# Performance work log

Hardware: AMD Instinct MI355X
Metric: run time of the kernel (lower is better)

Reference implementation:

```python
import jax, jax.numpy as jnp
import numpy as np

B, T, XS, HS = 256, 512, 256, 256


def setup_inputs() -> dict:
    key = jax.random.key(0)
    ks = jax.random.split(key, 9)
    scale_x = np.sqrt(6.0 / (XS + HS)).astype(np.float32)  # xavier_uniform-like scale
    scale_h = np.sqrt(6.0 / (HS + HS)).astype(np.float32)
    d = {"x": jax.random.normal(ks[0], (B, T, XS), dtype=jnp.float32)}
    names = ["i", "f", "g", "o"]
    for n, kx, kh in zip(names, ks[1:5], ks[5:9]):
        d[f"wx_{n}"] = jax.random.uniform(kx, (XS, HS), jnp.float32, -scale_x, scale_x)
        d[f"wh_{n}"] = jax.random.uniform(kh, (HS, HS), jnp.float32, -scale_h, scale_h)
        d[f"bx_{n}"] = jnp.zeros((HS,), jnp.float32)
        d[f"bh_{n}"] = jnp.zeros((HS,), jnp.float32)
    return d


def reference(x, wx_i, bx_i, wh_i, bh_i, wx_f, bx_f, wh_f, bh_f,
              wx_g, bx_g, wh_g, bh_g, wx_o, bx_o, wh_o, bh_o):
    bs, ts, xs = x.shape
    hs = wx_i.shape[1]
    # Fuse the 4 input projections and 4 hidden projections into 2 GEMMs
    # (identical math to 8 separate matmuls).
    Wx = jnp.concatenate([wx_i, wx_f, wx_g, wx_o], axis=1)      # [xs, 4hs]
    Wh = jnp.concatenate([wh_i, wh_f, wh_g, wh_o], axis=1)      # [hs, 4hs]
    b = jnp.concatenate([bx_i + bh_i, bx_f + bh_f, bx_g + bh_g, bx_o + bh_o])

    # Precompute all input projections in one big GEMM: [bs, ts, 4hs]
    x_proj = jnp.einsum('btx,xg->btg', x, Wx) + b

    def step(carry, xt_proj):
        h, c = carry
        gates = xt_proj + h @ Wh                      # [bs, 4hs]
        i_t = jax.nn.sigmoid(gates[:, 0 * hs:1 * hs])
        f_t = jax.nn.sigmoid(gates[:, 1 * hs:2 * hs])
        g_t = jnp.tanh(gates[:, 2 * hs:3 * hs])
        o_t = jax.nn.sigmoid(gates[:, 3 * hs:4 * hs])
        c_new = f_t * c + i_t * g_t
        h_new = o_t * jnp.tanh(c_new)
        return (h_new, c_new), None

    h0 = jnp.zeros((bs, hs), x.dtype)
    c0 = jnp.zeros((bs, hs), x.dtype)
    (h_t, c_t), _ = jax.lax.scan(step, (h0, c0), jnp.swapaxes(x_proj, 0, 1))
    return (h_t, c_t)
```

## Files before the change

### kernel.cpp

```cpp
#include <hip/hip_runtime.h>
#include <hip/hip_bf16.h>

#define BB   256
#define TT   512
#define XSZ  256
#define HSZ  256
#define GLDSW 132

typedef __bf16 bf16_t;
typedef __attribute__((ext_vector_type(8))) __bf16 bf16x8;
typedef __attribute__((ext_vector_type(4))) float  f32x4;

__device__ __forceinline__ float sigmoidf_(float v) { return 1.0f / (1.0f + __expf(-v)); }
__device__ __forceinline__ float tanhf_(float v)    { return 1.0f - 2.0f / (1.0f + __expf(2.0f * v)); }

__global__ void prep_bias(const float* bx0, const float* bh0, const float* bx1, const float* bh1,
                          const float* bx2, const float* bh2, const float* bx3, const float* bh3,
                          float* bias) {
  const float* bxs[4] = {bx0, bx1, bx2, bx3};
  const float* bhs[4] = {bh0, bh1, bh2, bh3};
  int g = blockIdx.x, c = threadIdx.x;
  bias[g * 256 + c] = bxs[g][c] + bhs[g][c];
}

__global__ void prep_wtf(const float* wx0, const float* wh0, const float* wx1, const float* wh1,
                         const float* wx2, const float* wh2, const float* wx3, const float* wh3,
                         bf16_t* Wtf) {
  const float* whs[4] = {wh0, wh1, wh2, wh3};
  const float* wxs[4] = {wx0, wx1, wx2, wx3};
  int id = blockIdx.x * 256 + threadIdx.x;
  int L  = id & 63;
  int kt = (id >> 6) & 15;
  int w  = (id >> 10) & 7;
  int j  = (id >> 13) & 7;
  int sec = w >> 1, half = w & 1;
  int c   = j * 32 + half * 16 + (L & 15);
  int k0  = kt * 32 + (L >> 4) * 8;
  const float* src = (k0 < 256) ? (whs[sec] + (size_t)k0 * 256 + c)
                                : (wxs[sec] + (size_t)(k0 - 256) * 256 + c);
  bf16x8 v;
#pragma unroll
  for (int i = 0; i < 8; ++i) v[i] = (__bf16)src[(size_t)i * 256];
  reinterpret_cast<bf16x8*>(Wtf)[id] = v;
}

__global__ void prep_xbf(const float* __restrict__ x, bf16_t* __restrict__ xb) {
  size_t id = (size_t)blockIdx.x * 256 + threadIdx.x;
  const float* p = x + id * 8;
  f32x4 lo = *reinterpret_cast<const f32x4*>(p);
  f32x4 hi = *reinterpret_cast<const f32x4*>(p + 4);
  bf16x8 v;
#pragma unroll
  for (int i = 0; i < 4; ++i) { v[i] = (__bf16)lo[i]; v[i + 4] = (__bf16)hi[i]; }
  reinterpret_cast<bf16x8*>(xb)[id] = v;
}

template <bool XBF>
__global__ __launch_bounds__(512, 2)
void lstm_seq(const void* __restrict__ xsrc, const bf16_t* __restrict__ Wtf,
              const float* __restrict__ bias, bf16_t* __restrict__ hbuf0,
              bf16_t* __restrict__ hbuf1, unsigned* __restrict__ flags,
              float* __restrict__ out)
{
  __shared__ __align__(16) char  bxlds[65536];
  __shared__ __align__(16) char  hxl[8192];
  __shared__ __align__(16) float glds[16 * GLDSW];

  const int tid  = threadIdx.x;
  const int w    = tid >> 6;
  const int lane = tid & 63;
  const int l15  = lane & 15, l4 = lane >> 4;
  const int bid  = blockIdx.x;
  const int g    = bid >> 3, j = bid & 7;
  const int b0   = g * 16;
  const int sec  = w >> 1, half = w & 1;
  const int C    = sec * 256 + j * 32 + half * 16 + l15;

  const float*  xf32 = (const float*)xsrc;
  const bf16_t* xbf  = (const bf16_t*)xsrc;

  const float bias_v = bias[C];

  const char* wbase = (const char*)Wtf + ((size_t)(j * 8 + w) * 16) * 1024 + lane * 16;
  bf16x8 Bh[8];
#pragma unroll
  for (int kt = 0; kt < 8; ++kt)
    Bh[kt] = *reinterpret_cast<const bf16x8*>(wbase + kt * 1024);
#pragma unroll
  for (int q = 0; q < 8; ++q) {
    bf16x8 v = *reinterpret_cast<const bf16x8*>(wbase + (8 + q) * 1024);
    *reinterpret_cast<bf16x8*>(bxlds + (w * 8 + q) * 1024 + lane * 16) = v;
  }
  __syncthreads();

  const int crow = tid >> 5;
  const int ccol = tid & 31;
  float cst = 0.f;

  f32x4 acc_x = {bias_v, bias_v, bias_v, bias_v};
  {
#pragma unroll
    for (int k8 = 0; k8 < 8; ++k8) {
      bf16x8 a;
      if constexpr (XBF) {
        a = *reinterpret_cast<const bf16x8*>(
            xbf + (size_t)(b0 + l15) * (TT * XSZ) + k8 * 32 + l4 * 8);
      } else {
        const float* xp = xf32 + (size_t)(b0 + l15) * (TT * XSZ) + k8 * 32 + l4 * 8;
        f32x4 lo = *reinterpret_cast<const f32x4*>(xp);
        f32x4 hi = *reinterpret_cast<const f32x4*>(xp + 4);
#pragma unroll
        for (int i = 0; i < 4; ++i) { a[i] = (__bf16)lo[i]; a[i + 4] = (__bf16)hi[i]; }
      }
      bf16x8 bx = *reinterpret_cast<const bf16x8*>(bxlds + (w * 8 + k8) * 1024 + lane * 16);
      acc_x = __builtin_amdgcn_mfma_f32_16x16x32_bf16(a, bx, acc_x, 0, 0, 0);
    }
  }

#pragma unroll 1
  for (int t = 0; t < TT; ++t) {
    f32x4 acc = acc_x;

    if (t > 0) {
      const unsigned* fp = flags + (size_t)(g * 8 + (lane & 7)) * 16;
      for (;;) {
        unsigned v;
        asm volatile("global_load_dword %0, %1, off sc0 sc1\n\t"
                     "s_waitcnt vmcnt(0)"
                     : "=v"(v) : "v"(fp) : "memory");
        if (__all((int)(v >= (unsigned)t))) break;
        __builtin_amdgcn_s_sleep(1);
      }
      __builtin_amdgcn_sched_barrier(0);

      const bf16_t* hb = (t & 1) ? hbuf1 : hbuf0;
      bf16x8 hch;
      const bf16_t* hp = hb + (size_t)(b0 + l15) * HSZ + w * 32 + l4 * 8;
      asm volatile("global_load_dwordx4 %0, %1, off sc0 sc1\n\t"
                   "s_waitcnt vmcnt(0)"
                   : "=v"(hch) : "v"(hp) : "memory");
      __builtin_amdgcn_sched_barrier(0);
      *reinterpret_cast<bf16x8*>(hxl + w * 1024 + lane * 16) = hch;
      __syncthreads();

#pragma unroll
      for (int kt = 0; kt < 8; ++kt) {
        bf16x8 a = *reinterpret_cast<const bf16x8*>(hxl + kt * 1024 + lane * 16);
        acc = __builtin_amdgcn_mfma_f32_16x16x32_bf16(a, Bh[kt], acc, 0, 0, 0);
      }
    }

    {
      const int col = sec * 32 + half * 16 + l15;
#pragma unroll
      for (int r = 0; r < 4; ++r)
        glds[(l4 * 4 + r) * GLDSW + col] = acc[r];
    }
    __syncthreads();

    const float* gp = &glds[crow * GLDSW + ccol];
    float i_t = sigmoidf_(gp[0]);
    float f_t = sigmoidf_(gp[32]);
    float g_t = tanhf_(gp[64]);
    float o_t = sigmoidf_(gp[96]);
    float cn  = f_t * cst + i_t * g_t;
    cst = cn;
    float hval = o_t * tanhf_(cn);

    if (t + 1 < TT) {
      __bf16 hb16 = (__bf16)hval;
      unsigned hv = (unsigned)__builtin_bit_cast(unsigned short, hb16);
      bf16_t* hp = ((t + 1) & 1 ? hbuf1 : hbuf0) + (size_t)(b0 + crow) * HSZ + j * 32 + ccol;
      asm volatile("global_store_short %0, %1, off sc0 sc1" :: "v"(hp), "v"(hv) : "memory");
      asm volatile("s_waitcnt vmcnt(0)" ::: "memory");
      __builtin_amdgcn_sched_barrier(0);
    } else {
      float* op = out + (size_t)(b0 + crow) * HSZ + j * 32 + ccol;
      op[0] = hval;
      op[(size_t)BB * HSZ] = cst;
    }
    __syncthreads();

    if (t + 1 < TT) {
      if (tid == 0) {
        unsigned fv = (unsigned)(t + 1);
        const unsigned* fp = &flags[(size_t)bid * 16];
        asm volatile("global_store_dword %0, %1, off sc0 sc1" :: "v"(fp), "v"(fv) : "memory");
      }

      acc_x = f32x4{bias_v, bias_v, bias_v, bias_v};
#pragma unroll
      for (int k8 = 0; k8 < 8; ++k8) {
        bf16x8 a;
        if constexpr (XBF) {
          a = *reinterpret_cast<const bf16x8*>(
              xbf + (size_t)(b0 + l15) * (TT * XSZ) + (size_t)(t + 1) * XSZ + k8 * 32 + l4 * 8);
        } else {
          const float* xp = xf32 + (size_t)(b0 + l15) * (TT * XSZ) + (size_t)(t + 1) * XSZ + k8 * 32 + l4 * 8;
          f32x4 lo = *reinterpret_cast<const f32x4*>(xp);
          f32x4 hi = *reinterpret_cast<const f32x4*>(xp + 4);
#pragma unroll
          for (int i = 0; i < 4; ++i) { a[i] = (__bf16)lo[i]; a[i + 4] = (__bf16)hi[i]; }
        }
        bf16x8 bx = *reinterpret_cast<const bf16x8*>(bxlds + (w * 8 + k8) * 1024 + lane * 16);
        acc_x = __builtin_amdgcn_mfma_f32_16x16x32_bf16(a, bx, acc_x, 0, 0, 0);
      }
    }
  }
}

extern "C" void kernel_launch(void* const* d_in, const int* in_sizes, int n_in,
                              void* d_out, int out_size, void* d_ws, size_t ws_size,
                              hipStream_t stream) {
  const float* x = (const float*)d_in[0];
  const float *wx[4], *wh[4], *bx[4], *bh[4];
  for (int g = 0; g < 4; ++g) {
    wx[g] = (const float*)d_in[1 + 4 * g];
    wh[g] = (const float*)d_in[2 + 4 * g];
    bx[g] = (const float*)d_in[3 + 4 * g];
    bh[g] = (const float*)d_in[4 + 4 * g];
  }

  char* ws = (char*)d_ws;
  unsigned* flags = (unsigned*)(ws);
  float*    bias  = (float*)(ws + 8192);
  bf16_t*   hbuf0 = (bf16_t*)(ws + 16384);
  bf16_t*   hbuf1 = (bf16_t*)(ws + 16384 + 131072);
  bf16_t*   Wtf   = (bf16_t*)(ws + 16384 + 262144);
  bf16_t*   xbf   = (bf16_t*)(ws + 16384 + 262144 + 1048576);
  const size_t need_xbf = 16384 + 262144 + 1048576 + (size_t)BB * TT * XSZ * 2;

  hipMemsetAsync(flags, 0, 8192, stream);

  prep_bias<<<dim3(4), dim3(256), 0, stream>>>(bx[0], bh[0], bx[1], bh[1],
                                               bx[2], bh[2], bx[3], bh[3], bias);
  prep_wtf<<<dim3(256), dim3(256), 0, stream>>>(wx[0], wh[0], wx[1], wh[1],
                                                wx[2], wh[2], wx[3], wh[3], Wtf);
  if (ws_size >= need_xbf) {
    prep_xbf<<<dim3((BB * TT * XSZ / 8) / 256), dim3(256), 0, stream>>>(x, xbf);
    lstm_seq<true><<<dim3(128), dim3(512), 0, stream>>>(xbf, Wtf, bias, hbuf0, hbuf1,
                                                        flags, (float*)d_out);
  } else {
    lstm_seq<false><<<dim3(128), dim3(512), 0, stream>>>(x, Wtf, bias, hbuf0, hbuf1,
                                                         flags, (float*)d_out);
  }
}
```

Measured before the change: 2.179 ms.

## Embed step tags in hidden-state words to replace separate flag polling

Each hidden value is now stored as a 32-bit word holding the bf16 value plus the timestep tag in the upper half. Consumers poll the data directly until every tag matches, which removes the separate flag store, the wait-for-store fence and one barrier per step. The LDS staging for h is double-buffered, and the next step's x rows are prefetched into registers before the spin wait. In exchange h traffic doubles in size, and correctness depends on the tag check being reliable without a memset, since stale workspace data could falsely match a tag.

```diff
diff --git a/kernel.cpp b/kernel.cpp
--- a/kernel.cpp
+++ b/kernel.cpp
@@ -10,6 +10,7 @@
 typedef __bf16 bf16_t;
 typedef __attribute__((ext_vector_type(8))) __bf16 bf16x8;
 typedef __attribute__((ext_vector_type(4))) float  f32x4;
+typedef __attribute__((ext_vector_type(4))) unsigned uint4v;
 
 __device__ __forceinline__ float sigmoidf_(float v) { return 1.0f / (1.0f + __expf(-v)); }
 __device__ __forceinline__ float tanhf_(float v)    { return 1.0f - 2.0f / (1.0f + __expf(2.0f * v)); }
@@ -58,12 +59,11 @@
 template <bool XBF>
 __global__ __launch_bounds__(512, 2)
 void lstm_seq(const void* __restrict__ xsrc, const bf16_t* __restrict__ Wtf,
-              const float* __restrict__ bias, bf16_t* __restrict__ hbuf0,
-              bf16_t* __restrict__ hbuf1, unsigned* __restrict__ flags,
+              const float* __restrict__ bias, unsigned* __restrict__ hseq,
               float* __restrict__ out)
 {
   __shared__ __align__(16) char  bxlds[65536];
-  __shared__ __align__(16) char  hxl[8192];
+  __shared__ __align__(16) char  hxl[2][8192];
   __shared__ __align__(16) float glds[16 * GLDSW];
 
   const int tid  = threadIdx.x;
@@ -98,54 +98,68 @@
   float cst = 0.f;
 
   f32x4 acc_x = {bias_v, bias_v, bias_v, bias_v};
-  {
-#pragma unroll
-    for (int k8 = 0; k8 < 8; ++k8) {
-      bf16x8 a;
-      if constexpr (XBF) {
-        a = *reinterpret_cast<const bf16x8*>(
-            xbf + (size_t)(b0 + l15) * (TT * XSZ) + k8 * 32 + l4 * 8);
-      } else {
-        const float* xp = xf32 + (size_t)(b0 + l15) * (TT * XSZ) + k8 * 32 + l4 * 8;
-        f32x4 lo = *reinterpret_cast<const f32x4*>(xp);
-        f32x4 hi = *reinterpret_cast<const f32x4*>(xp + 4);
-#pragma unroll
-        for (int i = 0; i < 4; ++i) { a[i] = (__bf16)lo[i]; a[i + 4] = (__bf16)hi[i]; }
-      }
-      bf16x8 bx = *reinterpret_cast<const bf16x8*>(bxlds + (w * 8 + k8) * 1024 + lane * 16);
-      acc_x = __builtin_amdgcn_mfma_f32_16x16x32_bf16(a, bx, acc_x, 0, 0, 0);
-    }
+#pragma unroll
+  for (int k8 = 0; k8 < 8; ++k8) {
+    bf16x8 a;
+    if constexpr (XBF) {
+      a = *reinterpret_cast<const bf16x8*>(
+          xbf + (size_t)(b0 + l15) * (TT * XSZ) + k8 * 32 + l4 * 8);
+    } else {
+      const float* xp = xf32 + (size_t)(b0 + l15) * (TT * XSZ) + k8 * 32 + l4 * 8;
+      f32x4 lo = *reinterpret_cast<const f32x4*>(xp);
+      f32x4 hi = *reinterpret_cast<const f32x4*>(xp + 4);
+#pragma unroll
+      for (int i = 0; i < 4; ++i) { a[i] = (__bf16)lo[i]; a[i + 4] = (__bf16)hi[i]; }
+    }
+    bf16x8 bx = *reinterpret_cast<const bf16x8*>(bxlds + (w * 8 + k8) * 1024 + lane * 16);
+    acc_x = __builtin_amdgcn_mfma_f32_16x16x32_bf16(a, bx, acc_x, 0, 0, 0);
   }
 
 #pragma unroll 1
   for (int t = 0; t < TT; ++t) {
     f32x4 acc = acc_x;
 
+    bf16x8 ax[8];
+    if constexpr (XBF) {
+      if (t + 1 < TT) {
+#pragma unroll
+        for (int k8 = 0; k8 < 8; ++k8)
+          ax[k8] = *reinterpret_cast<const bf16x8*>(
+              xbf + (size_t)(b0 + l15) * (TT * XSZ) + (size_t)(t + 1) * XSZ + k8 * 32 + l4 * 8);
+      }
+    }
+
     if (t > 0) {
-      const unsigned* fp = flags + (size_t)(g * 8 + (lane & 7)) * 16;
+      const unsigned* hp = hseq + (size_t)(t & 1) * 65536
+                         + (size_t)(b0 + l15) * HSZ + w * 32 + l4 * 8;
+      const unsigned tg = (unsigned)t;
+      uint4v A, B;
       for (;;) {
-        unsigned v;
-        asm volatile("global_load_dword %0, %1, off sc0 sc1\n\t"
+        asm volatile("global_load_dwordx4 %0, %2, off sc0 sc1\n\t"
+                     "global_load_dwordx4 %1, %2, off offset:16 sc0 sc1\n\t"
                      "s_waitcnt vmcnt(0)"
-                     : "=v"(v) : "v"(fp) : "memory");
-        if (__all((int)(v >= (unsigned)t))) break;
+                     : "=&v"(A), "=&v"(B) : "v"(hp) : "memory");
+        bool ok = ((A[0] >> 16) == tg) & ((A[1] >> 16) == tg) &
+                  ((A[2] >> 16) == tg) & ((A[3] >> 16) == tg) &
+                  ((B[0] >> 16) == tg) & ((B[1] >> 16) == tg) &
+                  ((B[2] >> 16) == tg) & ((B[3] >> 16) == tg);
+        if (__all((int)ok)) break;
         __builtin_amdgcn_s_sleep(1);
       }
       __builtin_amdgcn_sched_barrier(0);
-
-      const bf16_t* hb = (t & 1) ? hbuf1 : hbuf0;
-      bf16x8 hch;
-      const bf16_t* hp = hb + (size_t)(b0 + l15) * HSZ + w * 32 + l4 * 8;
-      asm volatile("global_load_dwordx4 %0, %1, off sc0 sc1\n\t"
-                   "s_waitcnt vmcnt(0)"
-                   : "=v"(hch) : "v"(hp) : "memory");
-      __builtin_amdgcn_sched_barrier(0);
-      *reinterpret_cast<bf16x8*>(hxl + w * 1024 + lane * 16) = hch;
-      __syncthreads();
-
+      unsigned p0 = (A[0] & 0xFFFFu) | (A[1] << 16);
+      unsigned p1 = (A[2] & 0xFFFFu) | (A[3] << 16);
+      unsigned p2 = (B[0] & 0xFFFFu) | (B[1] << 16);
+      unsigned p3 = (B[2] & 0xFFFFu) | (B[3] << 16);
+      uint4v pk = {p0, p1, p2, p3};
+      *reinterpret_cast<uint4v*>(hxl[t & 1] + w * 1024 + lane * 16) = pk;
+    }
+    __syncthreads();
+
+    if (t > 0) {
 #pragma unroll
       for (int kt = 0; kt < 8; ++kt) {
-        bf16x8 a = *reinterpret_cast<const bf16x8*>(hxl + kt * 1024 + lane * 16);
+        bf16x8 a = *reinterpret_cast<const bf16x8*>(hxl[t & 1] + kt * 1024 + lane * 16);
         acc = __builtin_amdgcn_mfma_f32_16x16x32_bf16(a, Bh[kt], acc, 0, 0, 0);
       }
     }
@@ -169,42 +183,33 @@
 
     if (t + 1 < TT) {
       __bf16 hb16 = (__bf16)hval;
-      unsigned hv = (unsigned)__builtin_bit_cast(unsigned short, hb16);
-      bf16_t* hp = ((t + 1) & 1 ? hbuf1 : hbuf0) + (size_t)(b0 + crow) * HSZ + j * 32 + ccol;
-      asm volatile("global_store_short %0, %1, off sc0 sc1" :: "v"(hp), "v"(hv) : "memory");
-      asm volatile("s_waitcnt vmcnt(0)" ::: "memory");
-      __builtin_amdgcn_sched_barrier(0);
+      unsigned hv = ((unsigned)(t + 1) << 16)
+                  | (unsigned)__builtin_bit_cast(unsigned short, hb16);
+      unsigned* hp = hseq + (size_t)((t + 1) & 1) * 65536
+                   + (size_t)(b0 + crow) * HSZ + j * 32 + ccol;
+      asm volatile("global_store_dword %0, %1, off sc0 sc1" :: "v"(hp), "v"(hv) : "memory");
+
+      acc_x = f32x4{bias_v, bias_v, bias_v, bias_v};
+#pragma unroll
+      for (int k8 = 0; k8 < 8; ++k8) {
+        bf16x8 a;
+        if constexpr (XBF) {
+          a = ax[k8];
+        } else {
+          const float* xp = xf32 + (size_t)(b0 + l15) * (TT * XSZ)
+                          + (size_t)(t + 1) * XSZ + k8 * 32 + l4 * 8;
+          f32x4 lo = *reinterpret_cast<const f32x4*>(xp);
+          f32x4 hi = *reinterpret_cast<const f32x4*>(xp + 4);
+#pragma unroll
+          for (int i = 0; i < 4; ++i) { a[i] = (__bf16)lo[i]; a[i + 4] = (__bf16)hi[i]; }
+        }
+        bf16x8 bx = *reinterpret_cast<const bf16x8*>(bxlds + (w * 8 + k8) * 1024 + lane * 16);
+        acc_x = __builtin_amdgcn_mfma_f32_16x16x32_bf16(a, bx, acc_x, 0, 0, 0);
+      }
     } else {
       float* op = out + (size_t)(b0 + crow) * HSZ + j * 32 + ccol;
       op[0] = hval;
       op[(size_t)BB * HSZ] = cst;
-    }
-    __syncthreads();
-
-    if (t + 1 < TT) {
-      if (tid == 0) {
-        unsigned fv = (unsigned)(t + 1);
-        const unsigned* fp = &flags[(size_t)bid * 16];
-        asm volatile("global_store_dword %0, %1, off sc0 sc1" :: "v"(fp), "v"(fv) : "memory");
-      }
-
-      acc_x = f32x4{bias_v, bias_v, bias_v, bias_v};
-#pragma unroll
-      for (int k8 = 0; k8 < 8; ++k8) {
-        bf16x8 a;
-        if constexpr (XBF) {
-          a = *reinterpret_cast<const bf16x8*>(
-              xbf + (size_t)(b0 + l15) * (TT * XSZ) + (size_t)(t + 1) * XSZ + k8 * 32 + l4 * 8);
-        } else {
-          const float* xp = xf32 + (size_t)(b0 + l15) * (TT * XSZ) + (size_t)(t + 1) * XSZ + k8 * 32 + l4 * 8;
-          f32x4 lo = *reinterpret_cast<const f32x4*>(xp);
-          f32x4 hi = *reinterpret_cast<const f32x4*>(xp + 4);
-#pragma unroll
-          for (int i = 0; i < 4; ++i) { a[i] = (__bf16)lo[i]; a[i + 4] = (__bf16)hi[i]; }
-        }
-        bf16x8 bx = *reinterpret_cast<const bf16x8*>(bxlds + (w * 8 + k8) * 1024 + lane * 16);
-        acc_x = __builtin_amdgcn_mfma_f32_16x16x32_bf16(a, bx, acc_x, 0, 0, 0);
-      }
     }
   }
 }
@@ -222,15 +227,11 @@
   }
 
   char* ws = (char*)d_ws;
-  unsigned* flags = (unsigned*)(ws);
-  float*    bias  = (float*)(ws + 8192);
-  bf16_t*   hbuf0 = (bf16_t*)(ws + 16384);
-  bf16_t*   hbuf1 = (bf16_t*)(ws + 16384 + 131072);
-  bf16_t*   Wtf   = (bf16_t*)(ws + 16384 + 262144);
-  bf16_t*   xbf   = (bf16_t*)(ws + 16384 + 262144 + 1048576);
-  const size_t need_xbf = 16384 + 262144 + 1048576 + (size_t)BB * TT * XSZ * 2;
-
-  hipMemsetAsync(flags, 0, 8192, stream);
+  float*    bias = (float*)ws;
+  bf16_t*   Wtf  = (bf16_t*)(ws + 4096);
+  unsigned* hseq = (unsigned*)(ws + 4096 + 1048576);
+  bf16_t*   xbf  = (bf16_t*)(ws + 4096 + 1048576 + 524288);
+  const size_t need_xbf = 4096 + 1048576 + 524288 + (size_t)BB * TT * XSZ * 2;
 
   prep_bias<<<dim3(4), dim3(256), 0, stream>>>(bx[0], bh[0], bx[1], bh[1],
                                                bx[2], bh[2], bx[3], bh[3], bias);
@@ -238,10 +239,10 @@
                                                 wx[2], wh[2], wx[3], wh[3], Wtf);
   if (ws_size >= need_xbf) {
     prep_xbf<<<dim3((BB * TT * XSZ / 8) / 256), dim3(256), 0, stream>>>(x, xbf);
-    lstm_seq<true><<<dim3(128), dim3(512), 0, stream>>>(xbf, Wtf, bias, hbuf0, hbuf1,
-                                                        flags, (float*)d_out);
+    lstm_seq<true><<<dim3(128), dim3(512), 0, stream>>>(xbf, Wtf, bias, hseq,
+                                                        (float*)d_out);
   } else {
-    lstm_seq<false><<<dim3(128), dim3(512), 0, stream>>>(x, Wtf, bias, hbuf0, hbuf1,
-                                                         flags, (float*)d_out);
-  }
-}
+    lstm_seq<false><<<dim3(128), dim3(512), 0, stream>>>(x, Wtf, bias, hseq,
+                                                         (float*)d_out);
+  }
+}
```

After: 1.861 ms, median of 2. 14.6% less time.
